# Performance work log

Hardware: AMD Instinct MI355X
Metric: run time of the kernel (lower is better)

The kernel has to match this reference:

```python
import jax, jax.numpy as jnp
import numpy as np

D = 256          # hidden_dim
H = 4            # num_heads
HD = D // H      # head_dim = 64
E = 4            # num_experts (hard-coded in MoE)
TOPK = 2         # top_k (hard-coded)
DFF = 2 * D      # expert ffn width
EPS = 1e-5


def _ln(x, g, b):
    mu = x.mean(-1, keepdims=True)
    var = x.var(-1, keepdims=True)  # biased, matches torch LayerNorm
    return (x - mu) * jax.lax.rsqrt(var + EPS) * g + b


def _ff(x, w1, b1, w2, b2):
    h = jax.nn.gelu(x @ w1 + b1, approximate=False)  # torch nn.GELU default = exact erf
    return h @ w2 + b2


def setup_inputs() -> dict:
    key = jax.random.key(0)
    ks = jax.random.split(key, 24)
    B, S, IN = 4, 2048, 256
    s = 0.02
    inp = {
        'x': jax.random.normal(ks[0], (B, S, IN), jnp.float32),
        'mask': jax.random.randint(ks[1], (B, S), 0, 2).astype(jnp.int32),
        'w_in': jax.random.normal(ks[2], (IN, D), jnp.float32) * s,
        'b_in': jnp.zeros((D,), jnp.float32),
        'g1': jnp.ones((D,), jnp.float32),
        'be1': jnp.zeros((D,), jnp.float32),
        'wq': jax.random.normal(ks[3], (D, D), jnp.float32) * s,
        'bq': jnp.zeros((D,), jnp.float32),
        'wk': jax.random.normal(ks[4], (D, D), jnp.float32) * s,
        'bk': jnp.zeros((D,), jnp.float32),
        'wv': jax.random.normal(ks[5], (D, D), jnp.float32) * s,
        'bv': jnp.zeros((D,), jnp.float32),
        'wo': jax.random.normal(ks[6], (D, D), jnp.float32) * s,
        'bo': jnp.zeros((D,), jnp.float32),
        'g2': jnp.ones((D,), jnp.float32),
        'be2': jnp.zeros((D,), jnp.float32),
        'wg': jax.random.normal(ks[7], (D, E), jnp.float32) * s,
        'bg': jnp.zeros((E,), jnp.float32),
        'ew1': jax.random.normal(ks[8], (E, D, DFF), jnp.float32) * s,
        'eb1': jnp.zeros((E, DFF), jnp.float32),
        'ew2': jax.random.normal(ks[9], (E, DFF, D), jnp.float32) * s,
        'eb2': jnp.zeros((E, D), jnp.float32),
    }
    return inp


def reference(x, mask, w_in, b_in, g1, be1, wq, bq, wk, bk, wv, bv, wo, bo, g2, be2, wg, bg, ew1, eb1, ew2, eb2):
    B, S, _ = x.shape
    x = x @ w_in + b_in
    res = x
    h = _ln(x, g1, be1)
    q = (h @ wq + bq).reshape(B, S, H, HD).transpose(0, 2, 1, 3)  # bhsd
    k = (h @ wk + bk).reshape(B, S, H, HD).transpose(0, 2, 1, 3)
    v = (h @ wv + bv).reshape(B, S, H, HD).transpose(0, 2, 1, 3)
    # RoPE (interleaved pairs, half-concat output, as in source)
    inv_freq = 1.0 / (10000.0 ** (jnp.arange(0, HD, 2, dtype=jnp.float32) / HD))
    ang = jnp.arange(S, dtype=jnp.float32)[:, None] * inv_freq[None, :]  # [S, HD//2]
    sin, cos = jnp.sin(ang), jnp.cos(ang)  # broadcast over (B,H)
    def rot(t):
        ts = t.reshape(B, H, S, HD // 2, 2)
        t0, t1 = ts[..., 0], ts[..., 1]
        return jnp.concatenate([t0 * cos - t1 * sin, t1 * cos + t0 * sin], axis=-1)
    qr, kr = rot(q), rot(k)
    attn = jnp.einsum('bhqd,bhkd->bhqk', qr, kr) * (HD ** -0.5)
    row = mask[:, None, :, None]  # [B,1,S,1] -> masks whole query rows
    attn = jnp.where(row == 0, jnp.float32(-1e4), attn)
    valid = (row * S).astype(jnp.float32)           # [B,1,S,1]
    all_masked = valid == 0
    uniform = jnp.where(row != 0, 1.0 / jnp.maximum(valid, 1.0), 0.0)
    attn = jnp.where(all_masked, uniform, attn)
    attn = jax.nn.softmax(attn, axis=-1)
    out = jnp.einsum('bhqk,bhkd->bhqd', attn, v).transpose(0, 2, 1, 3).reshape(B, S, D)
    out = out @ wo + bo
    x = res + out
    res2 = x
    h2 = _ln(x, g2, be2)
    # MoE (faithful: expert i only applied where top-k slot i picked expert i)
    gp = jax.nn.softmax(h2 @ wg + bg, axis=-1)
    topv, topi = jax.lax.top_k(gp, TOPK)
    moe_out = jnp.zeros_like(h2)
    for i in range(TOPK):
        eo = _ff(h2, ew1[i], eb1[i], ew2[i], eb2[i])
        m = (topi[..., i] == i)[..., None].astype(h2.dtype)
        moe_out = moe_out + m * eo * topv[..., i:i + 1]
    flat = topi.reshape(-1)
    total = sum((flat == i).sum() for i in range(TOPK)).astype(jnp.float32)
    usage = jnp.zeros((E,), jnp.float32) + total
    usage = usage / usage.sum()
    lb = (jnp.std(usage, ddof=1) / usage.mean()) ** 2
    y = res2 + h2  # source discards moe_out / lb (likely a bug); kept live with exact 0* add
    return y + 0.0 * (moe_out.sum() + lb)
```

## Files before the change

### kernel.cpp

```cpp
#include <hip/hip_runtime.h>
#include <cstddef>

#define Bb    4
#define Sq    2048
#define Dd    256
#define Hh    4
#define HDh   64
#define NROWS (Bb*Sq)
#define EPSf  1e-5f

typedef unsigned short u16;
typedef unsigned int   u32;
typedef unsigned long long u64;
typedef __attribute__((ext_vector_type(8))) short  frag_ab;
typedef __attribute__((ext_vector_type(4))) float  frag_cd;

__device__ __forceinline__ u16 f2bf(float f){
    union { float f; u32 u; } v; v.f = f;
    u32 r = v.u + 0x7fffu + ((v.u >> 16) & 1u);
    return (u16)(r >> 16);
}
__device__ __forceinline__ u16 f2bf_trunc(float f){
    union { float f; u32 u; } v; v.f = f;
    return (u16)(v.u >> 16);
}
__device__ __forceinline__ float bf2f(u32 u){
    union { u32 u; float f; } v; v.u = u << 16; return v.f;
}

__global__ __launch_bounds__(256) void k0_prep(
    const float* __restrict__ w_in, const float* __restrict__ wq,
    const float* __restrict__ wk,   const float* __restrict__ wv,
    const float* __restrict__ wo,
    u16* __restrict__ wT, float* __restrict__ tab)
{
    const int bid = blockIdx.x, tid = threadIdx.x;
    if (bid < 80){
        __shared__ float T[64][65];
        const int wsel = bid >> 4, tile = bid & 15;
        const int k0 = (tile >> 2) * 64, n0 = (tile & 3) * 64;
        const float* src = wsel==0 ? w_in : wsel==1 ? wq : wsel==2 ? wk
                         : wsel==3 ? wv : wo;
        #pragma unroll
        for (int i=0;i<16;++i){
            int idx = i*256 + tid, k = idx>>6, n = idx&63;
            T[k][n] = src[(size_t)(k0+k)*Dd + n0 + n];
        }
        __syncthreads();
        u16* dst = wT + (size_t)wsel*Dd*Dd;
        #pragma unroll
        for (int i=0;i<16;++i){
            int idx = i*256 + tid, n = idx>>6, k = idx&63;
            dst[(size_t)(n0+n)*Dd + k0 + k] = f2bf(T[k][n]);
        }
    } else {
        int s = (bid-80)*8 + (tid>>5);
        int p = tid & 31;
        float invf = exp2f(-(float)p * (13.287712379549449f/32.f));
        float sn, cs; sincosf((float)s * invf, &sn, &cs);
        tab[(size_t)s*64 + p]      = cs;
        tab[(size_t)s*64 + 32 + p] = sn;
    }
}

__global__ __launch_bounds__(512) void k1_fused(
    const float* __restrict__ x,  const float* __restrict__ tab,
    const u16* __restrict__ wTin, const u16* __restrict__ wTqkv,
    const float* __restrict__ b_in, const float* __restrict__ g1,
    const float* __restrict__ be1,  const float* __restrict__ bq,
    const float* __restrict__ bk,   const float* __restrict__ bv,
    float* __restrict__ x1, u16* __restrict__ qro,
    u16* __restrict__ kro,  u16* __restrict__ vto)
{
    const int tid  = threadIdx.x;
    const int w    = tid >> 6;
    const int lane = tid & 63;
    const int l16  = lane & 15;
    const int quad = lane >> 4;
    const int r0   = blockIdx.x * 32;
    const int b    = r0 >> 11;
    const int s0   = r0 & (Sq-1);

    __shared__ u16 Xs[32][264];
    __shared__ u16 Hs[32][264];
    __shared__ u16 Os[32][776];
    __shared__ float red[2][32][8];

    #pragma unroll
    for (int i=0;i<4;++i){
        int f = i*512 + tid;
        int row = f>>6, cc = f&63;
        float4 v4 = *(const float4*)(x + (size_t)(r0+row)*Dd + cc*4);
        u16 pk4[4] = { f2bf(v4.x), f2bf(v4.y), f2bf(v4.z), f2bf(v4.w) };
        *(u64*)&Xs[row][cc*4] = *(u64*)pk4;
    }
    __syncthreads();

    const int cA = w*32 + quad*4;
    frag_cd acc[2][2];
    #pragma unroll
    for (int nt=0;nt<2;++nt){
        float4 b4 = *(const float4*)&b_in[cA + nt*16];
        acc[0][nt] = (frag_cd){b4.x, b4.y, b4.z, b4.w};
        acc[1][nt] = acc[0][nt];
    }
    #pragma unroll
    for (int kc=0;kc<8;++kc){
        frag_ab xa0 = *(frag_ab*)&Xs[l16][kc*32 + quad*8];
        frag_ab xa1 = *(frag_ab*)&Xs[16+l16][kc*32 + quad*8];
        #pragma unroll
        for (int nt=0;nt<2;++nt){
            frag_ab wf = *(const frag_ab*)&wTin[(size_t)(w*32+nt*16+l16)*Dd + kc*32 + quad*8];
            acc[0][nt] = __builtin_amdgcn_mfma_f32_16x16x32_bf16(wf, xa0, acc[0][nt], 0,0,0);
            acc[1][nt] = __builtin_amdgcn_mfma_f32_16x16x32_bf16(wf, xa1, acc[1][nt], 0,0,0);
        }
    }

    #pragma unroll
    for (int rg=0;rg<2;++rg){
        float s=0.f, q=0.f;
        #pragma unroll
        for (int nt=0;nt<2;++nt){
            float4 v4 = make_float4(acc[rg][nt][0], acc[rg][nt][1],
                                    acc[rg][nt][2], acc[rg][nt][3]);
            *(float4*)&x1[(size_t)(r0+rg*16+l16)*Dd + cA + nt*16] = v4;
            s += v4.x+v4.y+v4.z+v4.w;
            q += v4.x*v4.x + v4.y*v4.y + v4.z*v4.z + v4.w*v4.w;
        }
        s += __shfl_xor(s,16); q += __shfl_xor(q,16);
        s += __shfl_xor(s,32); q += __shfl_xor(q,32);
        if (lane < 16){ red[0][rg*16+l16][w]=s; red[1][rg*16+l16][w]=q; }
    }
    __syncthreads();

    #pragma unroll
    for (int rg=0;rg<2;++rg){
        int row = rg*16 + l16;
        float s8=0.f, q8=0.f;
        #pragma unroll
        for (int j=0;j<8;++j){ s8 += red[0][row][j]; q8 += red[1][row][j]; }
        float mu = s8*(1.f/Dd), ms = q8*(1.f/Dd);
        float rstd = rsqrtf(ms - mu*mu + EPSf);
        #pragma unroll
        for (int nt=0;nt<2;++nt){
            float4 g4 = *(const float4*)&g1[cA + nt*16];
            float4 e4 = *(const float4*)&be1[cA + nt*16];
            u16 pk4[4] = { f2bf((acc[rg][nt][0]-mu)*rstd*g4.x + e4.x),
                           f2bf((acc[rg][nt][1]-mu)*rstd*g4.y + e4.y),
                           f2bf((acc[rg][nt][2]-mu)*rstd*g4.z + e4.z),
                           f2bf((acc[rg][nt][3]-mu)*rstd*g4.w + e4.w) };
            *(u64*)&Hs[rg*16+l16][cA + nt*16] = *(u64*)pk4;
        }
    }
    __syncthreads();

    frag_cd a2[2][6];
    #pragma unroll
    for (int nt=0;nt<6;++nt){
        int c0 = w*96 + nt*16;
        const float* bp = (c0 < 256) ? bq : (c0 < 512 ? bk : bv);
        int cc = (c0 & 255) + quad*4;
        float4 b4 = *(const float4*)&bp[cc];
        a2[0][nt] = (frag_cd){b4.x, b4.y, b4.z, b4.w};
        a2[1][nt] = a2[0][nt];
    }
    #pragma unroll
    for (int kc=0;kc<8;++kc){
        frag_ab ha0 = *(frag_ab*)&Hs[l16][kc*32 + quad*8];
        frag_ab ha1 = *(frag_ab*)&Hs[16+l16][kc*32 + quad*8];
        #pragma unroll
        for (int nt=0;nt<6;++nt){
            frag_ab wf = *(const frag_ab*)&wTqkv[(size_t)(w*96+nt*16+l16)*Dd + kc*32 + quad*8];
            a2[0][nt] = __builtin_amdgcn_mfma_f32_16x16x32_bf16(wf, ha0, a2[0][nt], 0,0,0);
            a2[1][nt] = __builtin_amdgcn_mfma_f32_16x16x32_bf16(wf, ha1, a2[1][nt], 0,0,0);
        }
    }
    #pragma unroll
    for (int rg=0;rg<2;++rg)
        #pragma unroll
        for (int nt=0;nt<6;++nt){
            u16 pk4[4] = { f2bf(a2[rg][nt][0]), f2bf(a2[rg][nt][1]),
                           f2bf(a2[rg][nt][2]), f2bf(a2[rg][nt][3]) };
            *(u64*)&Os[rg*16+l16][w*96 + nt*16 + quad*4] = *(u64*)pk4;
        }
    __syncthreads();

    {
        const int row  = tid >> 4;
        const int head = (tid >> 2) & 3;
        const int pq   = tid & 3;
        const int sidx = s0 + row;
        const float* tb = tab + (size_t)sidx*64;
        float4 c0 = *(const float4*)(tb + pq*8);
        float4 c1 = *(const float4*)(tb + pq*8 + 4);
        float4 sn0 = *(const float4*)(tb + 32 + pq*8);
        float4 sn1 = *(const float4*)(tb + 32 + pq*8 + 4);
        const float cAr[8] = {c0.x,c0.y,c0.z,c0.w,c1.x,c1.y,c1.z,c1.w};
        const float sAr[8] = {sn0.x,sn0.y,sn0.z,sn0.w,sn1.x,sn1.y,sn1.z,sn1.w};
        #pragma unroll
        for (int tt=0; tt<2; ++tt){
            const int cbase = tt*256 + head*64;
            u16* dst = (tt==0 ? qro : kro) + ((size_t)(b*Hh+head)*Sq + sidx)*HDh;
            u16 lo[8], hi[8];
            #pragma unroll
            for (int j=0;j<8;++j){
                int p = pq*8 + j;
                u32 pr = *(const u32*)&Os[row][cbase + 2*p];
                float t0 = bf2f(pr & 0xffffu), t1 = bf2f(pr >> 16);
                lo[j] = f2bf(t0*cAr[j] - t1*sAr[j]);
                hi[j] = f2bf(t1*cAr[j] + t0*sAr[j]);
            }
            *(float4*)(dst + pq*8)      = *(float4*)lo;
            *(float4*)(dst + 32 + pq*8) = *(float4*)hi;
        }
    }
    {
        const int head = tid >> 7, d = (tid >> 1) & 63, rg = tid & 1;
        u16 pk[16];
        #pragma unroll
        for (int j=0;j<16;++j) pk[j] = Os[rg*16+j][512 + head*64 + d];
        u16* dst = vto + ((size_t)(b*Hh+head)*HDh + d)*Sq + s0 + rg*16;
        *(float4*)dst     = *(float4*)pk;
        *(float4*)(dst+8) = *(float4*)&pk[8];
    }
}

__global__ __launch_bounds__(512) void k2_attn(
    const u16* __restrict__ qr, const u16* __restrict__ kr,
    const u16* __restrict__ vt, const int* __restrict__ mask,
    u16* __restrict__ Opart, float* __restrict__ lpart)
{
    const int tid = threadIdx.x;
    const int w   = tid >> 6;
    const int lane= tid & 63;
    const int l16 = lane & 15;
    const int quad= lane >> 4;
    const int qt  = blockIdx.x;
    const int bh  = blockIdx.y;
    const int ks  = blockIdx.z;
    const int b   = bh >> 2;
    const int q0  = qt * 128;

    __shared__ u16 Ks [64][72];
    __shared__ u16 Vts[64][72];
    __shared__ u16 Ps [8][16][72];

    const u16* qg = qr + ((size_t)bh*Sq + q0 + w*16 + l16)*HDh;
    frag_ab qf0 = *(const frag_ab*)(qg + quad*8);
    frag_ab qf1 = *(const frag_ab*)(qg + quad*8 + 32);

    const float mf2 = (mask[(size_t)b*Sq + q0 + w*16 + l16] != 0)
                    ? 0.125f*1.44269504f : 0.f;

    float lsum = 0.f;
    frag_cd O[4];
    #pragma unroll
    for (int d=0; d<4; ++d) O[d] = (frag_cd){0.f,0.f,0.f,0.f};

    const u16* kg0 = kr + ((size_t)bh*Sq + ks*512)*HDh;
    const u16* vg0 = vt + (size_t)bh*HDh*Sq + ks*512;

    const int srow = tid >> 3, spart = tid & 7;

    for (int kt=0; kt<8; ++kt){
        __syncthreads();
        const u16* kg = kg0 + (size_t)kt*64*HDh;
        const u16* vg = vg0 + kt*64;
        *(float4*)&Ks [srow][spart*8] = *(const float4*)(kg + srow*HDh + spart*8);
        *(float4*)&Vts[srow][spart*8] = *(const float4*)(vg + (size_t)srow*Sq + spart*8);
        __syncthreads();

        frag_cd sc[4];
        #pragma unroll
        for (int t=0;t<4;++t){
            frag_ab kf0 = *(frag_ab*)&Ks[t*16 + l16][quad*8];
            frag_ab kf1 = *(frag_ab*)&Ks[t*16 + l16][quad*8 + 32];
            frag_cd z = (frag_cd){0.f,0.f,0.f,0.f};
            z = __builtin_amdgcn_mfma_f32_16x16x32_bf16(kf0, qf0, z, 0,0,0);
            z = __builtin_amdgcn_mfma_f32_16x16x32_bf16(kf1, qf1, z, 0,0,0);
            sc[t] = z;
        }

        #pragma unroll
        for (int t=0;t<4;++t){
            float p0 = exp2f(sc[t][0]*mf2);
            float p1 = exp2f(sc[t][1]*mf2);
            float p2 = exp2f(sc[t][2]*mf2);
            float p3 = exp2f(sc[t][3]*mf2);
            lsum += p0+p1+p2+p3;
            u16 pk4[4] = { f2bf_trunc(p0), f2bf_trunc(p1),
                           f2bf_trunc(p2), f2bf_trunc(p3) };
            *(u64*)&Ps[w][l16][t*16 + quad*4] = *(u64*)pk4;
        }

        frag_ab pf0 = *(frag_ab*)&Ps[w][l16][quad*8];
        frag_ab pf1 = *(frag_ab*)&Ps[w][l16][quad*8 + 32];

        #pragma unroll
        for (int d=0; d<4; ++d){
            frag_ab vf0 = *(frag_ab*)&Vts[d*16 + l16][quad*8];
            frag_ab vf1 = *(frag_ab*)&Vts[d*16 + l16][quad*8 + 32];
            O[d] = __builtin_amdgcn_mfma_f32_16x16x32_bf16(vf0, pf0, O[d], 0,0,0);
            O[d] = __builtin_amdgcn_mfma_f32_16x16x32_bf16(vf1, pf1, O[d], 0,0,0);
        }
    }

    u16* Ob = Opart + (((size_t)ks*16 + bh)*Sq + q0 + w*16 + l16)*HDh;
    #pragma unroll
    for (int dt=0; dt<4; ++dt){
        u16 pk4[4] = { f2bf(O[dt][0]), f2bf(O[dt][1]),
                       f2bf(O[dt][2]), f2bf(O[dt][3]) };
        *(u64*)(Ob + dt*16 + quad*4) = *(u64*)pk4;
    }
    lsum += __shfl_xor(lsum,16);
    lsum += __shfl_xor(lsum,32);
    if (lane < 16)
        lpart[((size_t)ks*16 + bh)*Sq + q0 + w*16 + l16] = lsum;
}

__global__ __launch_bounds__(512) void k3_gemm_ln(
    const u16* __restrict__ Opart, const float* __restrict__ lpart,
    const u16* __restrict__ wTo,
    const float* __restrict__ bo, const float* __restrict__ x1,
    const float* __restrict__ g2, const float* __restrict__ be2,
    float* __restrict__ out)
{
    const int tid  = threadIdx.x;
    const int w    = tid >> 6;
    const int lane = tid & 63;
    const int l16  = lane & 15;
    const int quad = lane >> 4;
    const int r0   = blockIdx.x * 32;
    const int b    = r0 >> 11;
    const int s0   = r0 & (Sq-1);
    const int cA   = w*32 + quad*4;

    __shared__ u16 Ats[32][264];
    __shared__ float red[2][32][8];
    __shared__ float linv[4][32];

    const size_t LS = (size_t)16*Sq;
    if (tid < 128){
        int h = tid >> 5, r = tid & 31;
        size_t li = ((size_t)(b*Hh + h))*Sq + s0 + r;
        linv[h][r] = 1.f / (lpart[li] + lpart[LS + li]
                          + lpart[2*LS + li] + lpart[3*LS + li]);
    }
    __syncthreads();

    const size_t SPLIT = (size_t)16*Sq*HDh;
    #pragma unroll
    for (int i=0;i<4;++i){
        int idx = i*512 + tid;
        int h = idx >> 9, rem = idx & 511, row = rem >> 4, c = rem & 15;
        size_t base = (((size_t)(b*Hh + h))*Sq + s0 + row)*HDh + c*4;
        u64 p0 = *(const u64*)(Opart + base);
        u64 p1 = *(const u64*)(Opart + SPLIT + base);
        u64 p2 = *(const u64*)(Opart + 2*SPLIT + base);
        u64 p3 = *(const u64*)(Opart + 3*SPLIT + base);
        float li = linv[h][row];
        u16 pk[4];
        #pragma unroll
        for (int j=0;j<4;++j){
            float v = bf2f((u32)((p0 >> (16*j)) & 0xffffu))
                    + bf2f((u32)((p1 >> (16*j)) & 0xffffu))
                    + bf2f((u32)((p2 >> (16*j)) & 0xffffu))
                    + bf2f((u32)((p3 >> (16*j)) & 0xffffu));
            pk[j] = f2bf(v*li);
        }
        *(u64*)&Ats[row][h*64 + c*4] = *(u64*)pk;
    }
    __syncthreads();

    frag_cd acc[2][2];
    #pragma unroll
    for (int nt=0;nt<2;++nt){
        float4 b4 = *(const float4*)&bo[cA + nt*16];
        acc[0][nt] = (frag_cd){b4.x, b4.y, b4.z, b4.w};
        acc[1][nt] = acc[0][nt];
    }
    #pragma unroll
    for (int kc=0;kc<8;++kc){
        frag_ab aa0 = *(frag_ab*)&Ats[l16][kc*32 + quad*8];
        frag_ab aa1 = *(frag_ab*)&Ats[16+l16][kc*32 + quad*8];
        #pragma unroll
        for (int nt=0;nt<2;++nt){
            frag_ab wf = *(const frag_ab*)&wTo[(size_t)(w*32+nt*16+l16)*Dd + kc*32 + quad*8];
            acc[0][nt] = __builtin_amdgcn_mfma_f32_16x16x32_bf16(wf, aa0, acc[0][nt], 0,0,0);
            acc[1][nt] = __builtin_amdgcn_mfma_f32_16x16x32_bf16(wf, aa1, acc[1][nt], 0,0,0);
        }
    }

    #pragma unroll
    for (int rg=0;rg<2;++rg){
        float s=0.f, q=0.f;
        #pragma unroll
        for (int nt=0;nt<2;++nt){
            float4 r4 = *(const float4*)&x1[(size_t)(r0+rg*16+l16)*Dd + cA + nt*16];
            acc[rg][nt][0] += r4.x; acc[rg][nt][1] += r4.y;
            acc[rg][nt][2] += r4.z; acc[rg][nt][3] += r4.w;
            s += acc[rg][nt][0]+acc[rg][nt][1]+acc[rg][nt][2]+acc[rg][nt][3];
            q += acc[rg][nt][0]*acc[rg][nt][0] + acc[rg][nt][1]*acc[rg][nt][1]
               + acc[rg][nt][2]*acc[rg][nt][2] + acc[rg][nt][3]*acc[rg][nt][3];
        }
        s += __shfl_xor(s,16); q += __shfl_xor(q,16);
        s += __shfl_xor(s,32); q += __shfl_xor(q,32);
        if (lane < 16){ red[0][rg*16+l16][w]=s; red[1][rg*16+l16][w]=q; }
    }
    __syncthreads();

    #pragma unroll
    for (int rg=0;rg<2;++rg){
        int row = rg*16 + l16;
        float s8=0.f, q8=0.f;
        #pragma unroll
        for (int j=0;j<8;++j){ s8 += red[0][row][j]; q8 += red[1][row][j]; }
        float mu = s8*(1.f/Dd), ms = q8*(1.f/Dd);
        float rstd = rsqrtf(ms - mu*mu + EPSf);
        #pragma unroll
        for (int nt=0;nt<2;++nt){
            float4 g4 = *(const float4*)&g2[cA + nt*16];
            float4 e4 = *(const float4*)&be2[cA + nt*16];
            float4 o4;
            o4.x = acc[rg][nt][0] + (acc[rg][nt][0]-mu)*rstd*g4.x + e4.x;
            o4.y = acc[rg][nt][1] + (acc[rg][nt][1]-mu)*rstd*g4.y + e4.y;
            o4.z = acc[rg][nt][2] + (acc[rg][nt][2]-mu)*rstd*g4.z + e4.z;
            o4.w = acc[rg][nt][3] + (acc[rg][nt][3]-mu)*rstd*g4.w + e4.w;
            *(float4*)&out[(size_t)(r0+row)*Dd + cA + nt*16] = o4;
        }
    }
}

extern "C" void kernel_launch(void* const* d_in, const int* in_sizes, int n_in,
                              void* d_out, int out_size, void* d_ws, size_t ws_size,
                              hipStream_t stream)
{
    const float* x    = (const float*)d_in[0];
    const int*   mask = (const int*)  d_in[1];
    const float* w_in = (const float*)d_in[2];
    const float* b_in = (const float*)d_in[3];
    const float* g1   = (const float*)d_in[4];
    const float* be1  = (const float*)d_in[5];
    const float* wq   = (const float*)d_in[6];
    const float* bq   = (const float*)d_in[7];
    const float* wk   = (const float*)d_in[8];
    const float* bk   = (const float*)d_in[9];
    const float* wv   = (const float*)d_in[10];
    const float* bv   = (const float*)d_in[11];
    const float* wo   = (const float*)d_in[12];
    const float* bo   = (const float*)d_in[13];
    const float* g2   = (const float*)d_in[14];
    const float* be2  = (const float*)d_in[15];

    float* out = (float*)d_out;
    char*  wsb = (char*)d_ws;

    float* x1    = (float*)(wsb);
    float* tab   = (float*)(wsb + ( 8u<<20));
    u16*   qro   = (u16*)(wsb + (12u<<20));
    u16*   kro   = (u16*)(wsb + (16u<<20));
    u16*   vto   = (u16*)(wsb + (20u<<20));
    u16*   Opart = (u16*)(wsb + (24u<<20));
    float* lpart = (float*)(wsb + (40u<<20));
    u16*   wT    = (u16*)(wsb + (40u<<20) + (768u<<10));

    k0_prep<<<336, 256, 0, stream>>>(w_in, wq, wk, wv, wo, wT, tab);
    k1_fused<<<NROWS/32, 512, 0, stream>>>(
        x, tab, wT, wT + Dd*Dd,
        b_in, g1, be1, bq, bk, bv, x1, qro, kro, vto);
    k2_attn<<<dim3(Sq/128, Bb*Hh, 4), 512, 0, stream>>>(qro, kro, vto, mask, Opart, lpart);
    k3_gemm_ln<<<NROWS/32, 512, 0, stream>>>(Opart, lpart, wT + 4*Dd*Dd,
                                             bo, x1, g2, be2, out);
}
```

Baseline: 170.7 us.

## Store residual in bf16 and double query rows per attention block

The residual x1 passed from k1 to k3 is now stored as bf16 instead of fp32, which halves that intermediate's write and read traffic at some cost in precision. The attention kernel now handles 256 query rows per block, two row groups per wave. Each K/V tile staged in shared memory is therefore reused for twice as many queries, halving K/V global loads and block count. In exchange there are more registers per wave and half as many blocks (512), which may lower occupancy.

```diff
diff --git a/kernel.cpp b/kernel.cpp
--- a/kernel.cpp
+++ b/kernel.cpp
@@ -69,7 +69,7 @@
     const float* __restrict__ b_in, const float* __restrict__ g1,
     const float* __restrict__ be1,  const float* __restrict__ bq,
     const float* __restrict__ bk,   const float* __restrict__ bv,
-    float* __restrict__ x1, u16* __restrict__ qro,
+    u16* __restrict__ x1, u16* __restrict__ qro,
     u16* __restrict__ kro,  u16* __restrict__ vto)
 {
     const int tid  = threadIdx.x;
@@ -121,11 +121,12 @@
         float s=0.f, q=0.f;
         #pragma unroll
         for (int nt=0;nt<2;++nt){
-            float4 v4 = make_float4(acc[rg][nt][0], acc[rg][nt][1],
-                                    acc[rg][nt][2], acc[rg][nt][3]);
-            *(float4*)&x1[(size_t)(r0+rg*16+l16)*Dd + cA + nt*16] = v4;
-            s += v4.x+v4.y+v4.z+v4.w;
-            q += v4.x*v4.x + v4.y*v4.y + v4.z*v4.z + v4.w*v4.w;
+            float v0=acc[rg][nt][0], v1=acc[rg][nt][1],
+                  v2=acc[rg][nt][2], v3=acc[rg][nt][3];
+            u16 pk4[4] = { f2bf(v0), f2bf(v1), f2bf(v2), f2bf(v3) };
+            *(u64*)&x1[(size_t)(r0+rg*16+l16)*Dd + cA + nt*16] = *(u64*)pk4;
+            s += v0+v1+v2+v3;
+            q += v0*v0 + v1*v1 + v2*v2 + v3*v3;
         }
         s += __shfl_xor(s,16); q += __shfl_xor(q,16);
         s += __shfl_xor(s,32); q += __shfl_xor(q,32);
@@ -239,23 +240,29 @@
     const int bh  = blockIdx.y;
     const int ks  = blockIdx.z;
     const int b   = bh >> 2;
-    const int q0  = qt * 128;
+    const int q0  = qt * 256;
 
     __shared__ u16 Ks [64][72];
     __shared__ u16 Vts[64][72];
-    __shared__ u16 Ps [8][16][72];
-
-    const u16* qg = qr + ((size_t)bh*Sq + q0 + w*16 + l16)*HDh;
-    frag_ab qf0 = *(const frag_ab*)(qg + quad*8);
-    frag_ab qf1 = *(const frag_ab*)(qg + quad*8 + 32);
-
-    const float mf2 = (mask[(size_t)b*Sq + q0 + w*16 + l16] != 0)
-                    ? 0.125f*1.44269504f : 0.f;
-
-    float lsum = 0.f;
-    frag_cd O[4];
-    #pragma unroll
-    for (int d=0; d<4; ++d) O[d] = (frag_cd){0.f,0.f,0.f,0.f};
+    __shared__ u16 Ps [8][2][16][72];
+
+    frag_ab qf[2][2];
+    float mf2[2];
+    #pragma unroll
+    for (int rg=0;rg<2;++rg){
+        const u16* qg = qr + ((size_t)bh*Sq + q0 + rg*128 + w*16 + l16)*HDh;
+        qf[rg][0] = *(const frag_ab*)(qg + quad*8);
+        qf[rg][1] = *(const frag_ab*)(qg + quad*8 + 32);
+        mf2[rg] = (mask[(size_t)b*Sq + q0 + rg*128 + w*16 + l16] != 0)
+                ? 0.125f*1.44269504f : 0.f;
+    }
+
+    float lsum[2] = {0.f, 0.f};
+    frag_cd O[2][4];
+    #pragma unroll
+    for (int rg=0;rg<2;++rg)
+        #pragma unroll
+        for (int d=0; d<4; ++d) O[rg][d] = (frag_cd){0.f,0.f,0.f,0.f};
 
     const u16* kg0 = kr + ((size_t)bh*Sq + ks*512)*HDh;
     const u16* vg0 = vt + (size_t)bh*HDh*Sq + ks*512;
@@ -270,58 +277,65 @@
         *(float4*)&Vts[srow][spart*8] = *(const float4*)(vg + (size_t)srow*Sq + spart*8);
         __syncthreads();
 
-        frag_cd sc[4];
-        #pragma unroll
-        for (int t=0;t<4;++t){
-            frag_ab kf0 = *(frag_ab*)&Ks[t*16 + l16][quad*8];
-            frag_ab kf1 = *(frag_ab*)&Ks[t*16 + l16][quad*8 + 32];
-            frag_cd z = (frag_cd){0.f,0.f,0.f,0.f};
-            z = __builtin_amdgcn_mfma_f32_16x16x32_bf16(kf0, qf0, z, 0,0,0);
-            z = __builtin_amdgcn_mfma_f32_16x16x32_bf16(kf1, qf1, z, 0,0,0);
-            sc[t] = z;
-        }
-
-        #pragma unroll
-        for (int t=0;t<4;++t){
-            float p0 = exp2f(sc[t][0]*mf2);
-            float p1 = exp2f(sc[t][1]*mf2);
-            float p2 = exp2f(sc[t][2]*mf2);
-            float p3 = exp2f(sc[t][3]*mf2);
-            lsum += p0+p1+p2+p3;
-            u16 pk4[4] = { f2bf_trunc(p0), f2bf_trunc(p1),
-                           f2bf_trunc(p2), f2bf_trunc(p3) };
-            *(u64*)&Ps[w][l16][t*16 + quad*4] = *(u64*)pk4;
-        }
-
-        frag_ab pf0 = *(frag_ab*)&Ps[w][l16][quad*8];
-        frag_ab pf1 = *(frag_ab*)&Ps[w][l16][quad*8 + 32];
-
-        #pragma unroll
-        for (int d=0; d<4; ++d){
-            frag_ab vf0 = *(frag_ab*)&Vts[d*16 + l16][quad*8];
-            frag_ab vf1 = *(frag_ab*)&Vts[d*16 + l16][quad*8 + 32];
-            O[d] = __builtin_amdgcn_mfma_f32_16x16x32_bf16(vf0, pf0, O[d], 0,0,0);
-            O[d] = __builtin_amdgcn_mfma_f32_16x16x32_bf16(vf1, pf1, O[d], 0,0,0);
-        }
-    }
-
-    u16* Ob = Opart + (((size_t)ks*16 + bh)*Sq + q0 + w*16 + l16)*HDh;
-    #pragma unroll
-    for (int dt=0; dt<4; ++dt){
-        u16 pk4[4] = { f2bf(O[dt][0]), f2bf(O[dt][1]),
-                       f2bf(O[dt][2]), f2bf(O[dt][3]) };
-        *(u64*)(Ob + dt*16 + quad*4) = *(u64*)pk4;
-    }
-    lsum += __shfl_xor(lsum,16);
-    lsum += __shfl_xor(lsum,32);
-    if (lane < 16)
-        lpart[((size_t)ks*16 + bh)*Sq + q0 + w*16 + l16] = lsum;
+        #pragma unroll
+        for (int rg=0;rg<2;++rg){
+            frag_cd sc[4];
+            #pragma unroll
+            for (int t=0;t<4;++t){
+                frag_ab kf0 = *(frag_ab*)&Ks[t*16 + l16][quad*8];
+                frag_ab kf1 = *(frag_ab*)&Ks[t*16 + l16][quad*8 + 32];
+                frag_cd z = (frag_cd){0.f,0.f,0.f,0.f};
+                z = __builtin_amdgcn_mfma_f32_16x16x32_bf16(kf0, qf[rg][0], z, 0,0,0);
+                z = __builtin_amdgcn_mfma_f32_16x16x32_bf16(kf1, qf[rg][1], z, 0,0,0);
+                sc[t] = z;
+            }
+
+            #pragma unroll
+            for (int t=0;t<4;++t){
+                float p0 = exp2f(sc[t][0]*mf2[rg]);
+                float p1 = exp2f(sc[t][1]*mf2[rg]);
+                float p2 = exp2f(sc[t][2]*mf2[rg]);
+                float p3 = exp2f(sc[t][3]*mf2[rg]);
+                lsum[rg] += p0+p1+p2+p3;
+                u16 pk4[4] = { f2bf_trunc(p0), f2bf_trunc(p1),
+                               f2bf_trunc(p2), f2bf_trunc(p3) };
+                *(u64*)&Ps[w][rg][l16][t*16 + quad*4] = *(u64*)pk4;
+            }
+
+            frag_ab pf0 = *(frag_ab*)&Ps[w][rg][l16][quad*8];
+            frag_ab pf1 = *(frag_ab*)&Ps[w][rg][l16][quad*8 + 32];
+
+            #pragma unroll
+            for (int d=0; d<4; ++d){
+                frag_ab vf0 = *(frag_ab*)&Vts[d*16 + l16][quad*8];
+                frag_ab vf1 = *(frag_ab*)&Vts[d*16 + l16][quad*8 + 32];
+                O[rg][d] = __builtin_amdgcn_mfma_f32_16x16x32_bf16(vf0, pf0, O[rg][d], 0,0,0);
+                O[rg][d] = __builtin_amdgcn_mfma_f32_16x16x32_bf16(vf1, pf1, O[rg][d], 0,0,0);
+            }
+        }
+    }
+
+    #pragma unroll
+    for (int rg=0;rg<2;++rg){
+        u16* Ob = Opart + (((size_t)ks*16 + bh)*Sq + q0 + rg*128 + w*16 + l16)*HDh;
+        #pragma unroll
+        for (int dt=0; dt<4; ++dt){
+            u16 pk4[4] = { f2bf(O[rg][dt][0]), f2bf(O[rg][dt][1]),
+                           f2bf(O[rg][dt][2]), f2bf(O[rg][dt][3]) };
+            *(u64*)(Ob + dt*16 + quad*4) = *(u64*)pk4;
+        }
+        float s = lsum[rg];
+        s += __shfl_xor(s,16);
+        s += __shfl_xor(s,32);
+        if (lane < 16)
+            lpart[((size_t)ks*16 + bh)*Sq + q0 + rg*128 + w*16 + l16] = s;
+    }
 }
 
 __global__ __launch_bounds__(512) void k3_gemm_ln(
     const u16* __restrict__ Opart, const float* __restrict__ lpart,
     const u16* __restrict__ wTo,
-    const float* __restrict__ bo, const float* __restrict__ x1,
+    const float* __restrict__ bo, const u16* __restrict__ x1,
     const float* __restrict__ g2, const float* __restrict__ be2,
     float* __restrict__ out)
 {
@@ -396,9 +410,11 @@
         float s=0.f, q=0.f;
         #pragma unroll
         for (int nt=0;nt<2;++nt){
-            float4 r4 = *(const float4*)&x1[(size_t)(r0+rg*16+l16)*Dd + cA + nt*16];
-            acc[rg][nt][0] += r4.x; acc[rg][nt][1] += r4.y;
-            acc[rg][nt][2] += r4.z; acc[rg][nt][3] += r4.w;
+            u64 r8 = *(const u64*)&x1[(size_t)(r0+rg*16+l16)*Dd + cA + nt*16];
+            acc[rg][nt][0] += bf2f((u32)( r8        & 0xffffu));
+            acc[rg][nt][1] += bf2f((u32)((r8 >> 16) & 0xffffu));
+            acc[rg][nt][2] += bf2f((u32)((r8 >> 32) & 0xffffu));
+            acc[rg][nt][3] += bf2f((u32)((r8 >> 48) & 0xffffu));
             s += acc[rg][nt][0]+acc[rg][nt][1]+acc[rg][nt][2]+acc[rg][nt][3];
             q += acc[rg][nt][0]*acc[rg][nt][0] + acc[rg][nt][1]*acc[rg][nt][1]
                + acc[rg][nt][2]*acc[rg][nt][2] + acc[rg][nt][3]*acc[rg][nt][3];
@@ -455,7 +471,7 @@
     float* out = (float*)d_out;
     char*  wsb = (char*)d_ws;
 
-    float* x1    = (float*)(wsb);
+    u16*   x1    = (u16*)(wsb);
     float* tab   = (float*)(wsb + ( 8u<<20));
     u16*   qro   = (u16*)(wsb + (12u<<20));
     u16*   kro   = (u16*)(wsb + (16u<<20));
@@ -468,7 +484,7 @@
     k1_fused<<<NROWS/32, 512, 0, stream>>>(
         x, tab, wT, wT + Dd*Dd,
         b_in, g1, be1, bq, bk, bv, x1, qro, kro, vto);
-    k2_attn<<<dim3(Sq/128, Bb*Hh, 4), 512, 0, stream>>>(qro, kro, vto, mask, Opart, lpart);
+    k2_attn<<<dim3(Sq/256, Bb*Hh, 4), 512, 0, stream>>>(qro, kro, vto, mask, Opart, lpart);
     k3_gemm_ln<<<NROWS/32, 512, 0, stream>>>(Opart, lpart, wT + 4*Dd*Dd,
                                              bo, x1, g2, be2, out);
 }
```

New measurement: 169.1 us. Within noise of the previous version (-1.0%).
